# Kernel tuning notes

Measured on AMD Instinct MI355X. Metric: run time of the kernel, lower is better.

## Reference

```python
import jax, jax.numpy as jnp
import numpy as np

B, N, D, HID, S, NH = 2, 384, 768, 256, 64, 8


def layernorm(x, g, b, eps=1e-5):
    m = x.mean(-1, keepdims=True)
    v = ((x - m) ** 2).mean(-1, keepdims=True)
    return (x - m) * jax.lax.rsqrt(v + eps) * g + b


def setup_inputs() -> dict:
    key = jax.random.key(0)
    ks = jax.random.split(key, 32)
    r = lambda i, shp: jax.random.normal(ks[i], shp, dtype=jnp.float32) * 0.02
    inp = {
        'coordinates': jax.random.normal(ks[0], (B, N, 3), dtype=jnp.float32),
        'features': jax.random.normal(ks[1], (B, N, D), dtype=jnp.float32),
        'superpoint_labels': jax.random.randint(ks[2], (B, N), 0, S),
        # geometric_encoder: Linear(9,HID)-LN-ReLU-Linear(HID,D)-LN
        'ge_w1': r(3, (9, HID)), 'ge_b1': jnp.zeros((HID,)),
        'ge_g1': jnp.ones((HID,)), 'ge_be1': jnp.zeros((HID,)),
        'ge_w2': r(4, (HID, D)), 'ge_b2': jnp.zeros((D,)),
        'ge_g2': jnp.ones((D,)), 'ge_be2': jnp.zeros((D,)),
        # superpoint_aggregator: Linear(D,HID)-LN-ReLU-Linear(HID,D)-LN
        'ag_w1': r(5, (D, HID)), 'ag_b1': jnp.zeros((HID,)),
        'ag_g1': jnp.ones((HID,)), 'ag_be1': jnp.zeros((HID,)),
        'ag_w2': r(6, (HID, D)), 'ag_b2': jnp.zeros((D,)),
        'ag_g2': jnp.ones((D,)), 'ag_be2': jnp.zeros((D,)),
        # spatial_attention (MultiheadAttention, 8 heads)
        'wq': r(7, (D, D)), 'bq': jnp.zeros((D,)),
        'wk': r(8, (D, D)), 'bk': jnp.zeros((D,)),
        'wv': r(9, (D, D)), 'bv': jnp.zeros((D,)),
        'wo': r(10, (D, D)), 'bo': jnp.zeros((D,)),
    }
    return inp


def _forward(coordinates, features, superpoint_labels,
             ge_w1, ge_b1, ge_g1, ge_be1, ge_w2, ge_b2, ge_g2, ge_be2,
             ag_w1, ag_b1, ag_g1, ag_be1, ag_w2, ag_b2, ag_g2, ag_be2,
             wq, bq, wk, bk, wv, bv, wo, bo):
    # pairwise geometric relations: [B,N,N,9]
    rp = coordinates[:, :, None, :] - coordinates[:, None, :, :]
    dist = jnp.linalg.norm(rp, axis=-1, keepdims=True)
    rn = rp / jnp.maximum(dist, 1e-12)  # F.normalize semantics
    z = jnp.zeros_like(rn[..., 0])
    # torch loop writes channels (i*3+j-3): (0,1)->-2==3, (0,2)->-1==4, (1,2)->2; ch 0,1 stay zero
    ang = jnp.stack([z, z, rn[..., 1] * rn[..., 2],
                     rn[..., 0] * rn[..., 1], rn[..., 0] * rn[..., 2]], axis=-1)
    rel = jnp.concatenate([dist, rn, ang], axis=-1)
    h = jax.nn.relu(layernorm(rel @ ge_w1 + ge_b1, ge_g1, ge_be1))
    enc = layernorm(h @ ge_w2 + ge_b2, ge_g2, ge_be2)  # [B,N,N,D]
    geo_ctx = enc.mean(axis=2)  # [B,N,D]
    # per-superpoint scatter-mean (vectorized over all groups)
    oh = jax.nn.one_hot(superpoint_labels, S, dtype=features.dtype)  # [B,N,S]
    cnt = oh.sum(axis=1)  # [B,S]
    denom = jnp.maximum(cnt, 1.0)[..., None]
    mean_f = jnp.einsum('bns,bnd->bsd', oh, features) / denom
    mean_g = jnp.einsum('bns,bnd->bsd', oh, geo_ctx) / denom
    ah = jax.nn.relu(layernorm(mean_f @ ag_w1 + ag_b1, ag_g1, ag_be1))
    agg = layernorm(ah @ ag_w2 + ag_b2, ag_g2, ag_be2)
    combined = agg + mean_g  # [B,S,D]
    bidx = jnp.arange(B)[:, None]
    comb_g = combined[bidx, superpoint_labels]  # gather back [B,N,D]
    valid = (cnt[bidx, superpoint_labels] >= 2.0)[..., None]
    cw = 0.3  # consistency_weight
    enhanced = jnp.where(valid, (1.0 - cw) * features + cw * comb_g, features)
    # cross-attention: q=enhanced, k=v=geo_ctx
    dh = D // NH
    q = (enhanced @ wq + bq).reshape(B, N, NH, dh).transpose(0, 2, 1, 3)
    k = (geo_ctx @ wk + bk).reshape(B, N, NH, dh).transpose(0, 2, 1, 3)
    v = (geo_ctx @ wv + bv).reshape(B, N, NH, dh).transpose(0, 2, 1, 3)
    attn = jax.nn.softmax(jnp.einsum('bhqd,bhkd->bhqk', q, k) * (dh ** -0.5), axis=-1)
    o = jnp.einsum('bhqk,bhkd->bhqd', attn, v).transpose(0, 2, 1, 3).reshape(B, N, D)
    spatial = o @ wo + bo
    return enhanced + 0.5 * spatial


def reference(coordinates, features, superpoint_labels,
              ge_w1, ge_b1, ge_g1, ge_be1, ge_w2, ge_b2, ge_g2, ge_be2,
              ag_w1, ag_b1, ag_g1, ag_be1, ag_w2, ag_b2, ag_g2, ag_be2,
              wq, bq, wk, bk, wv, bv, wo, bo):
    return _forward(coordinates, features, superpoint_labels,
                    ge_w1, ge_b1, ge_g1, ge_be1, ge_w2, ge_b2, ge_g2, ge_be2,
                    ag_w1, ag_b1, ag_g1, ag_be1, ag_w2, ag_b2, ag_g2, ag_be2,
                    wq, bq, wk, bk, wv, bv, wo, bo)
```

## Files before the change

### kernel.cpp

```cpp
#include <hip/hip_runtime.h>
#include <hip/hip_bf16.h>
#include <stdint.h>
#include <stddef.h>

#define BB 2
#define NN 384
#define DD 768
#define HH 256
#define SS 64
#define NHH 8
#define DHH 96

typedef __attribute__((ext_vector_type(8))) short bf16x8;
typedef __attribute__((ext_vector_type(4))) float f32x4;

__device__ __forceinline__ float bits_f(unsigned short u){
  unsigned x = ((unsigned)u) << 16; float f; __builtin_memcpy(&f, &x, 4); return f;
}
__device__ __forceinline__ unsigned short f_bits(float a){
  unsigned x; __builtin_memcpy(&x, &a, 4);
  unsigned r = x + 0x7fffu + ((x >> 16) & 1u);
  return (unsigned short)(r >> 16);
}
__device__ __forceinline__ float lo_f(unsigned u){ unsigned x = u << 16; float f; __builtin_memcpy(&f,&x,4); return f; }
__device__ __forceinline__ float hi_f(unsigned u){ unsigned x = u & 0xffff0000u; float f; __builtin_memcpy(&f,&x,4); return f; }

__global__ __launch_bounds__(256) void k_prep(
    const float* __restrict__ w2, const float* __restrict__ w1g,
    const float* __restrict__ wq, const float* __restrict__ wk,
    const float* __restrict__ wv, const float* __restrict__ wo,
    const float* __restrict__ aw1, const float* __restrict__ aw2,
    float* __restrict__ zf, short* __restrict__ w2T, short* __restrict__ w2r,
    short* __restrict__ wqT, short* __restrict__ wkT, short* __restrict__ wvT,
    short* __restrict__ woT, short* __restrict__ w1t,
    short* __restrict__ agw1T, short* __restrict__ agw2T)
{
  __shared__ short tile[64*66];
  const int tid = threadIdx.x, blk = blockIdx.x;
  if (blk < 1549){
    int idx = blk*256 + tid;
    if (idx < 396416) zf[idx] = 0.f;
    return;
  }
  if (blk < 1597){
    int t = blk - 1549;
    int r0 = (t/12)*64, c0 = (t%12)*64;
    int g = tid >> 6, c = tid & 63;
    #pragma unroll
    for (int i=0;i<16;++i){
      int r = i*4 + g;
      tile[r*66 + c] = (short)f_bits(w2[(size_t)(r0+r)*768 + c0 + c]);
    }
    __syncthreads();
    #pragma unroll
    for (int i=0;i<16;++i){
      int cc = i*4 + g, rr = c;
      w2T[(size_t)(c0+cc)*256 + r0 + rr] = tile[rr*66 + cc];
    }
    return;
  }
  if (blk < 2365){
    int idx = (blk-1597)*256 + tid;
    w2r[idx] = (short)f_bits(w2[idx]);
    return;
  }
  if (blk < 2941){
    int t = blk - 2365;
    int mat = t / 144, tt = t % 144;
    const float* W = (mat==0)?wq:(mat==1)?wk:(mat==2)?wv:wo;
    short* T = (mat==0)?wqT:(mat==1)?wkT:(mat==2)?wvT:woT;
    int r0 = (tt/12)*64, c0 = (tt%12)*64;
    int g = tid >> 6, c = tid & 63;
    #pragma unroll
    for (int i=0;i<16;++i){
      int r = i*4 + g;
      tile[r*66 + c] = (short)f_bits(W[(size_t)(r0+r)*768 + c0 + c]);
    }
    __syncthreads();
    #pragma unroll
    for (int i=0;i<16;++i){
      int cc = i*4 + g, rr = c;
      T[(size_t)(c0+cc)*768 + r0 + rr] = tile[rr*66 + cc];
    }
    return;
  }
  if (blk < 2973){
    int idx = (blk-2941)*256 + tid;
    int c = idx >> 5, kk = idx & 31;
    w1t[idx] = (kk < 9) ? (short)f_bits(w1g[kk*256 + c]) : (short)0;
    return;
  }
  if (blk < 3021){
    int t = blk - 2973;
    int r0 = (t/4)*64, c0 = (t%4)*64;
    int g = tid >> 6, c = tid & 63;
    #pragma unroll
    for (int i=0;i<16;++i){
      int r = i*4 + g;
      tile[r*66 + c] = (short)f_bits(aw1[(size_t)(r0+r)*256 + c0 + c]);
    }
    __syncthreads();
    #pragma unroll
    for (int i=0;i<16;++i){
      int cc = i*4 + g, rr = c;
      agw1T[(size_t)(c0+cc)*768 + r0 + rr] = tile[rr*66 + cc];
    }
    return;
  }
  {
    int t = blk - 3021;
    int r0 = (t/12)*64, c0 = (t%12)*64;
    int g = tid >> 6, c = tid & 63;
    #pragma unroll
    for (int i=0;i<16;++i){
      int r = i*4 + g;
      tile[r*66 + c] = (short)f_bits(aw2[(size_t)(r0+r)*768 + c0 + c]);
    }
    __syncthreads();
    #pragma unroll
    for (int i=0;i<16;++i){
      int cc = i*4 + g, rr = c;
      agw2T[(size_t)(c0+cc)*256 + r0 + rr] = tile[rr*66 + cc];
    }
  }
}

__global__ __launch_bounds__(256) void k_gprep(const short* __restrict__ w2r,
                                               const float* __restrict__ b2,
                                               const short* __restrict__ w1t,
                                               const float* __restrict__ b1,
                                               short* __restrict__ Gm, float* __restrict__ gscal,
                                               float* __restrict__ g1s){
  __shared__ float b2s[768];
  __shared__ float red[8];
  const int tid = threadIdx.x, blk = blockIdx.x;
  if (blk < 64){
    const int wave = tid >> 6, lane = tid & 63, quad = lane >> 4, l16 = lane & 15;
    const int id = blk*4 + wave, ti = id >> 4, tj = id & 15;
    f32x4 acc = (f32x4){0.f,0.f,0.f,0.f};
    for (int ks = 0; ks < 24; ++ks){
      bf16x8 af = *(const bf16x8*)&w2r[(size_t)(ti*16 + l16)*768 + ks*32 + quad*8];
      bf16x8 bf = *(const bf16x8*)&w2r[(size_t)(tj*16 + l16)*768 + ks*32 + quad*8];
      acc = __builtin_amdgcn_mfma_f32_16x16x32_bf16(af, bf, acc, 0,0,0);
    }
    #pragma unroll
    for (int r = 0; r < 4; ++r)
      Gm[(ti*16 + quad*4 + r)*256 + tj*16 + l16] = (short)f_bits(acc[r]);
  } else if (blk == 64){
    for (int c = tid; c < 768; c += 256) b2s[c] = b2[c];
    __syncthreads();
    float sa = 0.f, wa = 0.f;
    const uint4* wr = (const uint4*)(w2r + (size_t)tid*768);
    #pragma unroll 4
    for (int kk = 0; kk < 96; ++kk){
      uint4 ww = wr[kk];
      const float* bp = &b2s[kk*8];
      float x0=lo_f(ww.x), x1=hi_f(ww.x), x2=lo_f(ww.y), x3=hi_f(ww.y);
      float x4=lo_f(ww.z), x5=hi_f(ww.z), x6=lo_f(ww.w), x7=hi_f(ww.w);
      sa += (x0+x1)+(x2+x3)+(x4+x5)+(x6+x7);
      wa += bp[0]*x0 + bp[1]*x1 + bp[2]*x2 + bp[3]*x3
          + bp[4]*x4 + bp[5]*x5 + bp[6]*x6 + bp[7]*x7;
    }
    Gm[256*256 + tid] = (short)f_bits(sa);
    Gm[257*256 + tid] = (short)f_bits(wa);
    #pragma unroll
    for (int rr = 258; rr < 288; ++rr) Gm[rr*256 + tid] = 0;
    float pb = 0.f, pbb = 0.f;
    for (int c = tid; c < 768; c += 256){ float bb = b2s[c]; pb += bb; pbb += bb*bb; }
    for (int m = 32; m >= 1; m >>= 1){ pb += __shfl_xor(pb,m); pbb += __shfl_xor(pbb,m); }
    if ((tid & 63) == 0){ red[tid>>6] = pb; red[4+(tid>>6)] = pbb; }
    __syncthreads();
    if (tid == 0){ gscal[0] = red[0]+red[1]+red[2]+red[3]; gscal[1] = red[4]+red[5]+red[6]+red[7]; }
  } else {
    const unsigned short* w1u = (const unsigned short*)w1t;
    if (tid < 81){
      int i = tid / 9, j = tid % 9;
      float acc = 0.f;
      for (int c = 0; c < 256; ++c)
        acc += bits_f(w1u[c*32 + i]) * bits_f(w1u[c*32 + j]);
      g1s[18 + tid] = acc;
    } else if (tid < 90){
      int i = tid - 81;
      float sa = 0.f, sb = 0.f;
      for (int c = 0; c < 256; ++c){
        float x = bits_f(w1u[c*32 + i]);
        sa += x; sb += x * b1[c];
      }
      g1s[i] = sa; g1s[9 + i] = sb;
    } else if (tid == 90){
      float pb = 0.f, pbb = 0.f;
      for (int c = 0; c < 256; ++c){ float bb = b1[c]; pb += bb; pbb += bb*bb; }
      g1s[99] = pb; g1s[100] = pbb;
    }
  }
}

__global__ __launch_bounds__(256, 3) void k_geo(
    const float* __restrict__ coord, const short* __restrict__ w1t,
    const float* __restrict__ b1g, const float* __restrict__ g1g, const float* __restrict__ be1g,
    const short* __restrict__ Gm, const float* __restrict__ gscal,
    const float* __restrict__ g1s, float* __restrict__ gv)
{
  __shared__ short relbf[64*36];
  __shared__ short h_bf[64*256];
  __shared__ float rmean[64], rrstd[64];
  __shared__ float msum[64], wbsum[64], qsum[64];

  const int tid = threadIdx.x;
  const int pair = blockIdx.x % 768;
  const int jt   = blockIdx.x / 768;
  const int j0 = jt * 64;
  const int b = pair / NN;

  if (tid < 64){
    int j = j0 + tid;
    float cix = coord[pair*3+0], ciy = coord[pair*3+1], ciz = coord[pair*3+2];
    float dx = cix - coord[(b*NN+j)*3+0];
    float dy = ciy - coord[(b*NN+j)*3+1];
    float dz = ciz - coord[(b*NN+j)*3+2];
    float dist = sqrtf(dx*dx + dy*dy + dz*dz);
    float inv = 1.f / fmaxf(dist, 1e-12f);
    float x = dx*inv, y = dy*inv, z = dz*inv;
    float rv[9];
    rv[0]=dist; rv[1]=x; rv[2]=y; rv[3]=z; rv[4]=0.f; rv[5]=0.f;
    rv[6]=y*z; rv[7]=x*y; rv[8]=x*z;
    short* rr = &relbf[tid*36];
    float rbf[9];
    #pragma unroll
    for (int k=0;k<9;++k){
      unsigned short hb = f_bits(rv[k]);
      rr[k] = (short)hb; rbf[k] = bits_f(hb);
    }
    #pragma unroll
    for (int k=9;k<32;++k) rr[k]=0;
    float s = g1s[99], ssq = g1s[100];
    #pragma unroll
    for (int i=0;i<9;++i){
      s += rbf[i]*g1s[i];
      ssq += 2.f*rbf[i]*g1s[9+i];
      #pragma unroll
      for (int jj=0;jj<9;++jj) ssq += rbf[i]*rbf[jj]*g1s[18+i*9+jj];
    }
    float mean = s*(1.f/256.f);
    float var  = ssq*(1.f/256.f) - mean*mean;
    rmean[tid] = mean; rrstd[tid] = rsqrtf(var + 1e-5f);
  } else if (tid < 128){
    qsum[tid-64] = 0.f;
  }
  __syncthreads();

  const int wave = tid >> 6, lane = tid & 63, quad = lane >> 4, l16 = lane & 15;

  {
    bf16x8 af[4];
    #pragma unroll
    for (int rb=0;rb<4;++rb)
      af[rb] = *(const bf16x8*)&relbf[(rb*16 + l16)*36 + quad*8];
    f32x4 hacc[4][4];
    #pragma unroll
    for (int ci=0;ci<4;++ci){
      int cb = wave*4 + ci;
      bf16x8 bfw = *(const bf16x8*)&w1t[(cb*16 + l16)*32 + quad*8];
      #pragma unroll
      for (int rb=0;rb<4;++rb)
        hacc[ci][rb] = __builtin_amdgcn_mfma_f32_16x16x32_bf16(af[rb], bfw, (f32x4){0.f,0.f,0.f,0.f}, 0,0,0);
    }
    f32x4 rmv[4], rsv[4];
    #pragma unroll
    for (int rb=0;rb<4;++rb){
      rmv[rb] = *(const f32x4*)&rmean[rb*16 + quad*4];
      rsv[rb] = *(const f32x4*)&rrstd[rb*16 + quad*4];
    }
    #pragma unroll
    for (int ci=0;ci<4;++ci){
      int col = (wave*4+ci)*16 + l16;
      float b1c = b1g[col], g1c = g1g[col], be1c = be1g[col];
      int chb = col >> 3, lo = col & 7;
      #pragma unroll
      for (int rb=0;rb<4;++rb){
        #pragma unroll
        for (int r=0;r<4;++r){
          int row = rb*16 + quad*4 + r;
          float hn = (hacc[ci][rb][r] + b1c - rmv[rb][r]) * rsv[rb][r] * g1c + be1c;
          h_bf[row*256 + ((chb + row)&31)*8 + lo] = (short)f_bits(fmaxf(hn, 0.f));
        }
      }
    }
  }
  __syncthreads();

  {
    f32x4 acc[4][4];
    #pragma unroll
    for (int ci=0;ci<4;++ci)
      #pragma unroll
      for (int rb=0;rb<4;++rb) acc[ci][rb] = (f32x4){0.f,0.f,0.f,0.f};
    f32x4 eacc[4];
    #pragma unroll
    for (int rb=0;rb<4;++rb) eacc[rb] = (f32x4){0.f,0.f,0.f,0.f};
    for (int ks=0;ks<8;++ks){
      bf16x8 a4[4];
      #pragma unroll
      for (int rb=0;rb<4;++rb){
        int row = rb*16 + l16;
        a4[rb] = *(const bf16x8*)&h_bf[row*256 + (((ks*4 + quad) + row)&31)*8];
      }
      #pragma unroll
      for (int ci=0;ci<4;++ci){
        int n = (wave*4+ci)*16 + l16;
        bf16x8 bg = *(const bf16x8*)&Gm[n*256 + ks*32 + quad*8];
        #pragma unroll
        for (int rb=0;rb<4;++rb)
          acc[ci][rb] = __builtin_amdgcn_mfma_f32_16x16x32_bf16(a4[rb], bg, acc[ci][rb], 0,0,0);
      }
      if (wave == 0){
        bf16x8 bge = *(const bf16x8*)&Gm[(256 + l16)*256 + ks*32 + quad*8];
        #pragma unroll
        for (int rb=0;rb<4;++rb)
          eacc[rb] = __builtin_amdgcn_mfma_f32_16x16x32_bf16(a4[rb], bge, eacc[rb], 0,0,0);
      }
    }
    if (wave == 0 && l16 < 2){
      float* dst = (l16 == 0) ? msum : wbsum;
      #pragma unroll
      for (int rb=0;rb<4;++rb)
        #pragma unroll
        for (int r=0;r<4;++r) dst[rb*16 + quad*4 + r] = eacc[rb][r];
    }
    #pragma unroll
    for (int rb=0;rb<4;++rb){
      #pragma unroll
      for (int r=0;r<4;++r){
        int row = rb*16 + quad*4 + r;
        float qp = 0.f;
        #pragma unroll
        for (int ci=0;ci<4;++ci){
          int col = (wave*4+ci)*16 + l16;
          float hv = bits_f((unsigned short)h_bf[row*256 + (((col>>3)+row)&31)*8 + (col&7)]);
          qp += acc[ci][rb][r] * hv;
        }
        qp += __shfl_xor(qp,1);
        qp += __shfl_xor(qp,2);
        qp += __shfl_xor(qp,4);
        qp += __shfl_xor(qp,8);
        if (l16 == 0) atomicAdd(&qsum[row], qp);
      }
    }
  }
  __syncthreads();
  if (tid < 64){
    float Sb = gscal[0], Sbb = gscal[1];
    float m2 = (msum[tid] + Sb)*(1.f/768.f);
    float ssq = qsum[tid] + 2.f*wbsum[tid] + Sbb;
    float var = ssq*(1.f/768.f) - m2*m2;
    rmean[tid] = m2; rrstd[tid] = rsqrtf(var + 1e-5f);
  }
  __syncthreads();
  if (tid < 64){
    float rr = rrstd[tid], tt = rmean[tid]*rrstd[tid];
    for (int m = 32; m >= 1; m >>= 1){ rr += __shfl_xor(rr,m); tt += __shfl_xor(tt,m); }
    if (tid == 0){
      atomicAdd(&gv[pair*260 + 256], rr);
      atomicAdd(&gv[pair*260 + 257], tt);
    }
  }
  {
    const int cg = tid >> 3, jg = tid & 7;
    float vacc[8];
    #pragma unroll
    for (int e=0;e<8;++e) vacc[e] = 0.f;
    #pragma unroll
    for (int jj = 0; jj < 8; ++jj){
      int j = jg*8 + jj;
      bf16x8 hv8 = *(const bf16x8*)&h_bf[j*256 + ((cg + j)&31)*8];
      float r = rrstd[j];
      #pragma unroll
      for (int e=0;e<8;++e) vacc[e] += r * bits_f((unsigned short)hv8[e]);
    }
    #pragma unroll
    for (int e=0;e<8;++e){
      vacc[e] += __shfl_xor(vacc[e],1);
      vacc[e] += __shfl_xor(vacc[e],2);
      vacc[e] += __shfl_xor(vacc[e],4);
    }
    if (jg == 0){
      #pragma unroll
      for (int e=0;e<8;++e) atomicAdd(&gv[pair*260 + cg*8 + e], vacc[e]);
    }
  }
}

__global__ __launch_bounds__(256) void k_geoscat(
    const float* __restrict__ gv, const short* __restrict__ w2r,
    const float* __restrict__ b2g, const float* __restrict__ g2g,
    const float* __restrict__ be2g, unsigned short* __restrict__ geo,
    const int* __restrict__ lab, const float* __restrict__ feat,
    float* __restrict__ mf, float* __restrict__ mg, float* __restrict__ cntw){
  __shared__ float V[256];
  __shared__ float RT[2];
  const int tid = threadIdx.x, pair = blockIdx.x;
  V[tid] = gv[pair*260 + tid];
  if (tid < 2) RT[tid] = gv[pair*260 + 256 + tid];
  __syncthreads();
  float R = RT[0], T = RT[1];
  const unsigned short* wr = (const unsigned short*)w2r;
  float a0 = 0.f, a1 = 0.f, a2 = 0.f;
  #pragma unroll 4
  for (int k = 0; k < 256; ++k){
    float vk = V[k];
    const unsigned short* row = wr + (size_t)k*768;
    a0 += vk * bits_f(row[tid]);
    a1 += vk * bits_f(row[tid+256]);
    a2 += vk * bits_f(row[tid+512]);
  }
  size_t base = (size_t)pair*DD;
  unsigned short r0 = f_bits(g2g[tid]    *(a0 + b2g[tid]    *R - T)*(1.f/384.f) + be2g[tid]);
  unsigned short r1 = f_bits(g2g[tid+256]*(a1 + b2g[tid+256]*R - T)*(1.f/384.f) + be2g[tid+256]);
  unsigned short r2 = f_bits(g2g[tid+512]*(a2 + b2g[tid+512]*R - T)*(1.f/384.f) + be2g[tid+512]);
  geo[base + tid]       = r0;
  geo[base + tid + 256] = r1;
  geo[base + tid + 512] = r2;
  const int b = pair / NN;
  const int s = lab[pair];
  const size_t sb = (size_t)(b*SS + s)*DD;
  if (tid == 0) atomicAdd(&cntw[b*SS + s], 1.0f);
  atomicAdd(&mf[sb + tid],       feat[base + tid]);
  atomicAdd(&mf[sb + tid + 256], feat[base + tid + 256]);
  atomicAdd(&mf[sb + tid + 512], feat[base + tid + 512]);
  atomicAdd(&mg[sb + tid],       bits_f(r0));
  atomicAdd(&mg[sb + tid + 256], bits_f(r1));
  atomicAdd(&mg[sb + tid + 512], bits_f(r2));
}

__global__ __launch_bounds__(256) void k_agg(
    const float* __restrict__ mf, const float* __restrict__ mg,
    const float* __restrict__ cntw,
    const short* __restrict__ w1T, const float* __restrict__ b1g,
    const float* __restrict__ g1g, const float* __restrict__ be1g,
    const short* __restrict__ w2T, const float* __restrict__ b2g,
    const float* __restrict__ g2g, const float* __restrict__ be2g,
    float* __restrict__ comb)
{
  __shared__ float xr[DD];
  __shared__ float hr[HH];
  __shared__ float red[8];
  const int tid = threadIdx.x;
  const size_t base = (size_t)blockIdx.x * DD;
  const float inv = 1.f / fmaxf(cntw[blockIdx.x], 1.f);
  for (int c = tid; c < DD; c += 256) xr[c] = mf[base + c]*inv;
  __syncthreads();
  float a = b1g[tid];
  {
    const uint4* wr = (const uint4*)(w1T + (size_t)tid*768);
    #pragma unroll 4
    for (int kk = 0; kk < 96; ++kk){
      uint4 ww = wr[kk];
      const float* xp = &xr[kk*8];
      a += xp[0]*lo_f(ww.x) + xp[1]*hi_f(ww.x)
         + xp[2]*lo_f(ww.y) + xp[3]*hi_f(ww.y)
         + xp[4]*lo_f(ww.z) + xp[5]*hi_f(ww.z)
         + xp[6]*lo_f(ww.w) + xp[7]*hi_f(ww.w);
    }
  }
  float s = a, q = a*a;
  for (int m = 32; m >= 1; m >>= 1){ s += __shfl_xor(s,m); q += __shfl_xor(q,m); }
  if ((tid & 63) == 0){ red[tid>>6] = s; red[4+(tid>>6)] = q; }
  __syncthreads();
  s = red[0]+red[1]+red[2]+red[3]; q = red[4]+red[5]+red[6]+red[7];
  float mean = s*(1.f/HH), var = q*(1.f/HH) - mean*mean, rstd = rsqrtf(var + 1e-5f);
  float h = fmaxf((a-mean)*rstd*g1g[tid] + be1g[tid], 0.f);
  hr[tid] = h;
  __syncthreads();
  float a2[3];
  #pragma unroll
  for (int u = 0; u < 3; ++u){
    int c = tid + 256*u;
    float t = b2g[c];
    const uint4* wr = (const uint4*)(w2T + (size_t)c*256);
    #pragma unroll 4
    for (int kk = 0; kk < 32; ++kk){
      uint4 ww = wr[kk];
      const float* hp = &hr[kk*8];
      t += hp[0]*lo_f(ww.x) + hp[1]*hi_f(ww.x)
         + hp[2]*lo_f(ww.y) + hp[3]*hi_f(ww.y)
         + hp[4]*lo_f(ww.z) + hp[5]*hi_f(ww.z)
         + hp[6]*lo_f(ww.w) + hp[7]*hi_f(ww.w);
    }
    a2[u] = t;
  }
  float s2 = a2[0]+a2[1]+a2[2], q2 = a2[0]*a2[0]+a2[1]*a2[1]+a2[2]*a2[2];
  for (int m = 32; m >= 1; m >>= 1){ s2 += __shfl_xor(s2,m); q2 += __shfl_xor(q2,m); }
  __syncthreads();
  if ((tid & 63) == 0){ red[tid>>6] = s2; red[4+(tid>>6)] = q2; }
  __syncthreads();
  s2 = red[0]+red[1]+red[2]+red[3]; q2 = red[4]+red[5]+red[6]+red[7];
  float mean2 = s2*(1.f/DD), rstd2 = rsqrtf(q2*(1.f/DD) - mean2*mean2 + 1e-5f);
  #pragma unroll
  for (int u = 0; u < 3; ++u){
    int c = tid + 256*u;
    comb[base + c] = (a2[u]-mean2)*rstd2*g2g[c] + be2g[c] + mg[base + c]*inv;
  }
}

__global__ void k_enhance(const float* __restrict__ feat, const int* __restrict__ lab,
                          const float* __restrict__ cntw, const float* __restrict__ comb,
                          float* __restrict__ enh, unsigned short* __restrict__ enhb)
{
  int idx = blockIdx.x * 256 + threadIdx.x;
  int c = idx % DD; int bn = idx / DD; int b = bn / NN;
  int l = lab[bn];
  float f = feat[idx];
  float cg = comb[(size_t)(b*SS + l)*DD + c];
  float cnt = cntw[b*SS + l];
  float e = (cnt >= 2.0f) ? (0.7f*f + 0.3f*cg) : f;
  enh[idx] = e;
  enhb[idx] = f_bits(e);
}

__global__ __launch_bounds__(256, 4) void k_qkv(
    const unsigned short* __restrict__ enhb, const unsigned short* __restrict__ geo,
    const short* __restrict__ wqT, const short* __restrict__ wkT, const short* __restrict__ wvT,
    const float* __restrict__ bq, const float* __restrict__ bk, const float* __restrict__ bv,
    unsigned short* __restrict__ qo, unsigned short* __restrict__ ko, unsigned short* __restrict__ vo)
{
  const int tid = threadIdx.x, blk = blockIdx.x;
  const int m = blk / 144, rem = blk % 144;
  const int rt = rem / 3, ct = rem % 3;
  const int wave = tid >> 6, lane = tid & 63, quad = lane >> 4, l16 = lane & 15;
  const short* WT = (m==0)?wqT:(m==1)?wkT:wvT;
  const float* Bv = (m==0)?bq:(m==1)?bk:bv;
  unsigned short* Y = (m==0)?qo:(m==1)?ko:vo;
  const short* X = (const short*)((m==0)? enhb : geo);
  const float oscale = (m==0)? 0.10206207261596577f : 1.0f;
  const int row0 = rt*16;
  const int col0 = ct*256 + wave*64;

  f32x4 acc[4];
  #pragma unroll
  for (int cb=0;cb<4;++cb) acc[cb] = (f32x4){0.f,0.f,0.f,0.f};
  for (int ks = 0; ks < 24; ++ks){
    bf16x8 af = *(const bf16x8*)&X[(size_t)(row0 + l16)*DD + ks*32 + quad*8];
    #pragma unroll
    for (int cb=0;cb<4;++cb){
      bf16x8 bw = *(const bf16x8*)&WT[(size_t)(col0 + cb*16 + l16)*DD + ks*32 + quad*8];
      acc[cb] = __builtin_amdgcn_mfma_f32_16x16x32_bf16(af, bw, acc[cb], 0,0,0);
    }
  }
  #pragma unroll
  for (int cb=0;cb<4;++cb){
    int col = col0 + cb*16 + l16;
    float bb = Bv[col];
    #pragma unroll
    for (int r=0;r<4;++r){
      int row = row0 + quad*4 + r;
      Y[(size_t)row*DD + col] = f_bits((acc[cb][r] + bb)*oscale);
    }
  }
}

__global__ __launch_bounds__(256) void k_attn_split(
    const unsigned short* __restrict__ qws, const unsigned short* __restrict__ kws,
    const unsigned short* __restrict__ vws, float* __restrict__ pws)
{
  __shared__ short kt[64*104];
  __shared__ short vt[64*104];
  __shared__ float st[32*66];
  __shared__ float lsum[32];
  const int tid = threadIdx.x;
  const int half = blockIdx.x / 192;
  const int inner = blockIdx.x % 192;
  const int b = inner / (NHH*12); int rem = inner % (NHH*12);
  const int h = rem / 12; const int qt = rem % 12; const int q0 = qt*32;
  const int sq = tid >> 3, jp = tid & 7;
  const int qp = tid >> 4, dp = tid & 15;
  unsigned qreg[48];
  {
    const unsigned* qr = (const unsigned*)(qws + (size_t)(b*NN + q0 + sq)*DD + h*DHH);
    #pragma unroll
    for (int d2 = 0; d2 < 48; ++d2) qreg[d2] = qr[d2];
  }
  if (tid < 32) lsum[tid] = 0.f;
  float Oacc[2][6];
  #pragma unroll
// ... 153 lines not shown
      }
    }
  }
  __syncthreads();
  float l0 = 1.f / lsum[2*qp], l1 = 1.f / lsum[2*qp+1];
  size_t ob = (size_t)(b*NN + q0)*DD + h*DHH + dp*6;
  #pragma unroll
  for (int m = 0; m < 6; ++m){
    ows[ob + (size_t)(2*qp)*DD + m]   = f_bits(Oacc[0][m]*l0);
    ows[ob + (size_t)(2*qp+1)*DD + m] = f_bits(Oacc[1][m]*l1);
  }
}

__global__ __launch_bounds__(256, 4) void k_out(
    const unsigned short* __restrict__ ows, const float* __restrict__ enh,
    const short* __restrict__ woT, const float* __restrict__ bo, float* __restrict__ out)
{
  const int tid = threadIdx.x, blk = blockIdx.x;
  const int rt = blk / 3, ct = blk % 3;
  const int wave = tid >> 6, lane = tid & 63, quad = lane >> 4, l16 = lane & 15;
  const int row0 = rt*16;
  const int col0 = ct*256 + wave*64;
  f32x4 acc[4];
  #pragma unroll
  for (int cb=0;cb<4;++cb) acc[cb] = (f32x4){0.f,0.f,0.f,0.f};
  for (int ks = 0; ks < 24; ++ks){
    bf16x8 af = *(const bf16x8*)&((const short*)ows)[(size_t)(row0 + l16)*DD + ks*32 + quad*8];
    #pragma unroll
    for (int cb=0;cb<4;++cb){
      bf16x8 bw = *(const bf16x8*)&woT[(size_t)(col0 + cb*16 + l16)*DD + ks*32 + quad*8];
      acc[cb] = __builtin_amdgcn_mfma_f32_16x16x32_bf16(af, bw, acc[cb], 0,0,0);
    }
  }
  #pragma unroll
  for (int cb=0;cb<4;++cb){
    int col = col0 + cb*16 + l16;
    float bb = bo[col];
    #pragma unroll
    for (int r=0;r<4;++r){
      size_t idx = (size_t)(row0 + quad*4 + r)*DD + col;
      out[idx] = enh[idx] + 0.5f*(acc[cb][r] + bb);
    }
  }
}

extern "C" void kernel_launch(void* const* d_in, const int* in_sizes, int n_in,
                              void* d_out, int out_size, void* d_ws, size_t ws_size,
                              hipStream_t stream) {
  const float* coord = (const float*)d_in[0];
  const float* feat  = (const float*)d_in[1];
  const int*   lab   = (const int*)d_in[2];
  const float* ge_w1 = (const float*)d_in[3];
  const float* ge_b1 = (const float*)d_in[4];
  const float* ge_g1 = (const float*)d_in[5];
  const float* ge_be1= (const float*)d_in[6];
  const float* ge_w2 = (const float*)d_in[7];
  const float* ge_b2 = (const float*)d_in[8];
  const float* ge_g2 = (const float*)d_in[9];
  const float* ge_be2= (const float*)d_in[10];
  const float* ag_w1 = (const float*)d_in[11];
  const float* ag_b1 = (const float*)d_in[12];
  const float* ag_g1 = (const float*)d_in[13];
  const float* ag_be1= (const float*)d_in[14];
  const float* ag_w2 = (const float*)d_in[15];
  const float* ag_b2 = (const float*)d_in[16];
  const float* ag_g2 = (const float*)d_in[17];
  const float* ag_be2= (const float*)d_in[18];
  const float* wq = (const float*)d_in[19];
  const float* bq = (const float*)d_in[20];
  const float* wk = (const float*)d_in[21];
  const float* bk = (const float*)d_in[22];
  const float* wv = (const float*)d_in[23];
  const float* bv = (const float*)d_in[24];
  const float* wo = (const float*)d_in[25];
  const float* bo = (const float*)d_in[26];

  char* w = (char*)d_ws;
  unsigned short* geo_bf = (unsigned short*)(w);
  float*          enh_f  = (float*)(w + 1179648);
  unsigned short* enh_bf = (unsigned short*)(w + 3538944);
  unsigned short* qw_bf  = (unsigned short*)(w + 4718592);
  unsigned short* kw_bf  = (unsigned short*)(w + 5898240);
  unsigned short* vw_bf  = (unsigned short*)(w + 7077888);
  float*          gv     = (float*)(w + 8257536);
  float*          mf     = (float*)(w + 9056256);
  float*          mg     = (float*)(w + 9449472);
  float*          cntw   = (float*)(w + 9842688);
  float*          comb   = (float*)(w + 9843200);
  short*          w2T    = (short*)(w + 10236416);
  short*          w2r    = (short*)(w + 10629632);
  short*          w1t    = (short*)(w + 11022848);
  short*          Gm     = (short*)(w + 11039232);
  float*          g1s    = (float*)(w + 11186688);
  float*          gscal  = (float*)(w + 11187200);
  short*          wqT    = (short*)(w + 11187456);
  short*          wkT    = (short*)(w + 12367104);
  short*          wvT    = (short*)(w + 13546752);
  short*          woT    = (short*)(w + 14726400);
  short*          agw1T  = (short*)(w + 15906048);
  short*          agw2T  = (short*)(w + 16299264);
  float*          pws    = (float*)(w + 16692480);
  unsigned short* ow_bf  = geo_bf;
  const bool split_attn = (ws_size >= 21460224);

  hipLaunchKernelGGL(k_prep,    dim3(3069),  dim3(256), 0, stream,
                     ge_w2, ge_w1, wq, wk, wv, wo, ag_w1, ag_w2,
                     gv, w2T, w2r, wqT, wkT, wvT, woT, w1t, agw1T, agw2T);
  hipLaunchKernelGGL(k_gprep,   dim3(66),    dim3(256), 0, stream,
                     w2r, ge_b2, w1t, ge_b1, Gm, gscal, g1s);
  hipLaunchKernelGGL(k_geo,     dim3(4608),  dim3(256), 0, stream,
                     coord, w1t, ge_b1, ge_g1, ge_be1, Gm, gscal, g1s, gv);
  hipLaunchKernelGGL(k_geoscat, dim3(768),   dim3(256), 0, stream,
                     gv, w2r, ge_b2, ge_g2, ge_be2, geo_bf, lab, feat, mf, mg, cntw);
  hipLaunchKernelGGL(k_agg,     dim3(128),   dim3(256), 0, stream,
                     mf, mg, cntw, agw1T, ag_b1, ag_g1, ag_be1, agw2T, ag_b2, ag_g2, ag_be2, comb);
  hipLaunchKernelGGL(k_enhance, dim3(2304),  dim3(256), 0, stream,
                     feat, lab, cntw, comb, enh_f, enh_bf);
  hipLaunchKernelGGL(k_qkv,     dim3(432),   dim3(256), 0, stream,
                     enh_bf, geo_bf, wqT, wkT, wvT, bq, bk, bv, qw_bf, kw_bf, vw_bf);
  if (split_attn){
    hipLaunchKernelGGL(k_attn_split, dim3(384), dim3(256), 0, stream,
                       qw_bf, kw_bf, vw_bf, pws);
    hipLaunchKernelGGL(k_attnfin,    dim3(192), dim3(256), 0, stream,
                       pws, ow_bf);
  } else {
    hipLaunchKernelGGL(k_attn_full,  dim3(192), dim3(256), 0, stream,
                       qw_bf, kw_bf, vw_bf, ow_bf);
  }
  hipLaunchKernelGGL(k_out,     dim3(144),   dim3(256), 0, stream,
                     ow_bf, enh_f, woT, bo, (float*)d_out);
}
```

Baseline: 426.9 us.

## Fuse geo scatter into k_geo, replace atomic superpoint sums with gather in k_agg

k_geo now runs one block per point pair-row and loops over all six j-tiles inside the block, keeping the reductions in registers and shared memory. It then applies the w2 projection and LayerNorm directly, which removes the gv zero-fill, the global atomics and the separate k_geoscat launch. k_agg now builds the per-superpoint feature and geo means itself by scanning the labels, replacing the atomic scatter into mf/mg/cntw. The cost is fewer blocks for k_geo (768 instead of 4608), which lowers parallelism, and a serial scan over 384 points in each k_agg block.

Result: slower. 922.7 us (+116.2%).

```diff
diff --git a/kernel.cpp b/kernel.cpp
--- a/kernel.cpp
+++ b/kernel.cpp
@@ -30,20 +30,15 @@
     const float* __restrict__ wq, const float* __restrict__ wk,
     const float* __restrict__ wv, const float* __restrict__ wo,
     const float* __restrict__ aw1, const float* __restrict__ aw2,
-    float* __restrict__ zf, short* __restrict__ w2T, short* __restrict__ w2r,
+    short* __restrict__ w2T, short* __restrict__ w2r,
     short* __restrict__ wqT, short* __restrict__ wkT, short* __restrict__ wvT,
     short* __restrict__ woT, short* __restrict__ w1t,
     short* __restrict__ agw1T, short* __restrict__ agw2T)
 {
   __shared__ short tile[64*66];
   const int tid = threadIdx.x, blk = blockIdx.x;
-  if (blk < 1549){
-    int idx = blk*256 + tid;
-    if (idx < 396416) zf[idx] = 0.f;
-    return;
-  }
-  if (blk < 1597){
-    int t = blk - 1549;
+  if (blk < 48){
+    int t = blk;
     int r0 = (t/12)*64, c0 = (t%12)*64;
     int g = tid >> 6, c = tid & 63;
     #pragma unroll
@@ -59,13 +54,13 @@
     }
     return;
   }
-  if (blk < 2365){
-    int idx = (blk-1597)*256 + tid;
+  if (blk < 816){
+    int idx = (blk-48)*256 + tid;
     w2r[idx] = (short)f_bits(w2[idx]);
     return;
   }
-  if (blk < 2941){
-    int t = blk - 2365;
+  if (blk < 1392){
+    int t = blk - 816;
     int mat = t / 144, tt = t % 144;
     const float* W = (mat==0)?wq:(mat==1)?wk:(mat==2)?wv:wo;
     short* T = (mat==0)?wqT:(mat==1)?wkT:(mat==2)?wvT:woT;
@@ -84,14 +79,14 @@
     }
     return;
   }
-  if (blk < 2973){
-    int idx = (blk-2941)*256 + tid;
+  if (blk < 1424){
+    int idx = (blk-1392)*256 + tid;
     int c = idx >> 5, kk = idx & 31;
     w1t[idx] = (kk < 9) ? (short)f_bits(w1g[kk*256 + c]) : (short)0;
     return;
   }
-  if (blk < 3021){
-    int t = blk - 2973;
+  if (blk < 1472){
+    int t = blk - 1424;
     int r0 = (t/4)*64, c0 = (t%4)*64;
     int g = tid >> 6, c = tid & 63;
     #pragma unroll
@@ -108,7 +103,7 @@
     return;
   }
   {
-    int t = blk - 3021;
+    int t = blk - 1472;
     int r0 = (t/12)*64, c0 = (t%12)*64;
     int g = tid >> 6, c = tid & 63;
     #pragma unroll
@@ -199,176 +194,179 @@
     const float* __restrict__ coord, const short* __restrict__ w1t,
     const float* __restrict__ b1g, const float* __restrict__ g1g, const float* __restrict__ be1g,
     const short* __restrict__ Gm, const float* __restrict__ gscal,
-    const float* __restrict__ g1s, float* __restrict__ gv)
+    const float* __restrict__ g1s, const short* __restrict__ w2r,
+    const float* __restrict__ b2g, const float* __restrict__ g2g,
+    const float* __restrict__ be2g, unsigned short* __restrict__ geo)
 {
   __shared__ short relbf[64*36];
   __shared__ short h_bf[64*256];
   __shared__ float rmean[64], rrstd[64];
   __shared__ float msum[64], wbsum[64], qsum[64];
+  __shared__ float Vsh[256];
+  __shared__ float RT[2];
 
   const int tid = threadIdx.x;
-  const int pair = blockIdx.x % 768;
-  const int jt   = blockIdx.x / 768;
-  const int j0 = jt * 64;
+  const int pair = blockIdx.x;
   const int b = pair / NN;
-
+  const int wave = tid >> 6, lane = tid & 63, quad = lane >> 4, l16 = lane & 15;
+  const int cg = tid >> 3, jg = tid & 7;
+
+  float cix = 0.f, ciy = 0.f, ciz = 0.f;
   if (tid < 64){
-    int j = j0 + tid;
-    float cix = coord[pair*3+0], ciy = coord[pair*3+1], ciz = coord[pair*3+2];
-    float dx = cix - coord[(b*NN+j)*3+0];
-    float dy = ciy - coord[(b*NN+j)*3+1];
-    float dz = ciz - coord[(b*NN+j)*3+2];
-    float dist = sqrtf(dx*dx + dy*dy + dz*dz);
-    float inv = 1.f / fmaxf(dist, 1e-12f);
-    float x = dx*inv, y = dy*inv, z = dz*inv;
-    float rv[9];
-    rv[0]=dist; rv[1]=x; rv[2]=y; rv[3]=z; rv[4]=0.f; rv[5]=0.f;
-    rv[6]=y*z; rv[7]=x*y; rv[8]=x*z;
-    short* rr = &relbf[tid*36];
-    float rbf[9];
-    #pragma unroll
-    for (int k=0;k<9;++k){
-      unsigned short hb = f_bits(rv[k]);
-      rr[k] = (short)hb; rbf[k] = bits_f(hb);
-    }
-    #pragma unroll
-    for (int k=9;k<32;++k) rr[k]=0;
-    float s = g1s[99], ssq = g1s[100];
-    #pragma unroll
-    for (int i=0;i<9;++i){
-      s += rbf[i]*g1s[i];
-      ssq += 2.f*rbf[i]*g1s[9+i];
-      #pragma unroll
-      for (int jj=0;jj<9;++jj) ssq += rbf[i]*rbf[jj]*g1s[18+i*9+jj];
-    }
-    float mean = s*(1.f/256.f);
-    float var  = ssq*(1.f/256.f) - mean*mean;
-    rmean[tid] = mean; rrstd[tid] = rsqrtf(var + 1e-5f);
-  } else if (tid < 128){
-    qsum[tid-64] = 0.f;
-  }
-  __syncthreads();
-
-  const int wave = tid >> 6, lane = tid & 63, quad = lane >> 4, l16 = lane & 15;
-
-  {
-    bf16x8 af[4];
-    #pragma unroll
-    for (int rb=0;rb<4;++rb)
-      af[rb] = *(const bf16x8*)&relbf[(rb*16 + l16)*36 + quad*8];
-    f32x4 hacc[4][4];
-    #pragma unroll
-    for (int ci=0;ci<4;++ci){
-      int cb = wave*4 + ci;
-      bf16x8 bfw = *(const bf16x8*)&w1t[(cb*16 + l16)*32 + quad*8];
+    cix = coord[pair*3+0]; ciy = coord[pair*3+1]; ciz = coord[pair*3+2];
+  }
+  const float Sb = gscal[0], Sbb = gscal[1];
+  float vacc[8];
+  #pragma unroll
+  for (int e=0;e<8;++e) vacc[e] = 0.f;
+  float Racc = 0.f, Tacc = 0.f;
+
+  for (int jt = 0; jt < 6; ++jt){
+    const int j0 = jt * 64;
+    if (tid < 64){
+      int j = j0 + tid;
+      float dx = cix - coord[(b*NN+j)*3+0];
+      float dy = ciy - coord[(b*NN+j)*3+1];
+      float dz = ciz - coord[(b*NN+j)*3+2];
+      float dist = sqrtf(dx*dx + dy*dy + dz*dz);
+      float inv = 1.f / fmaxf(dist, 1e-12f);
+      float x = dx*inv, y = dy*inv, z = dz*inv;
+      float rv[9];
+      rv[0]=dist; rv[1]=x; rv[2]=y; rv[3]=z; rv[4]=0.f; rv[5]=0.f;
+      rv[6]=y*z; rv[7]=x*y; rv[8]=x*z;
+      short* rr = &relbf[tid*36];
+      float rbf[9];
+      #pragma unroll
+      for (int k=0;k<9;++k){
+        unsigned short hb = f_bits(rv[k]);
+        rr[k] = (short)hb; rbf[k] = bits_f(hb);
+      }
+      #pragma unroll
+      for (int k=9;k<32;++k) rr[k]=0;
+      float s = g1s[99], ssq = g1s[100];
+      #pragma unroll
+      for (int i=0;i<9;++i){
+        s += rbf[i]*g1s[i];
+        ssq += 2.f*rbf[i]*g1s[9+i];
+        #pragma unroll
+        for (int jj=0;jj<9;++jj) ssq += rbf[i]*rbf[jj]*g1s[18+i*9+jj];
+      }
+      float mean = s*(1.f/256.f);
+      float var  = ssq*(1.f/256.f) - mean*mean;
+      rmean[tid] = mean; rrstd[tid] = rsqrtf(var + 1e-5f);
+    } else if (tid < 128){
+      qsum[tid-64] = 0.f;
+    }
+    __syncthreads();
+
+    {
+      bf16x8 af[4];
       #pragma unroll
       for (int rb=0;rb<4;++rb)
-        hacc[ci][rb] = __builtin_amdgcn_mfma_f32_16x16x32_bf16(af[rb], bfw, (f32x4){0.f,0.f,0.f,0.f}, 0,0,0);
-    }
-    f32x4 rmv[4], rsv[4];
-    #pragma unroll
-    for (int rb=0;rb<4;++rb){
-      rmv[rb] = *(const f32x4*)&rmean[rb*16 + quad*4];
-      rsv[rb] = *(const f32x4*)&rrstd[rb*16 + quad*4];
-    }
-    #pragma unroll
-    for (int ci=0;ci<4;++ci){
-      int col = (wave*4+ci)*16 + l16;
-      float b1c = b1g[col], g1c = g1g[col], be1c = be1g[col];
-      int chb = col >> 3, lo = col & 7;
+        af[rb] = *(const bf16x8*)&relbf[(rb*16 + l16)*36 + quad*8];
+      f32x4 hacc[4][4];
+      #pragma unroll
+      for (int ci=0;ci<4;++ci){
+        int cb = wave*4 + ci;
+        bf16x8 bfw = *(const bf16x8*)&w1t[(cb*16 + l16)*32 + quad*8];
+        #pragma unroll
+        for (int rb=0;rb<4;++rb)
+          hacc[ci][rb] = __builtin_amdgcn_mfma_f32_16x16x32_bf16(af[rb], bfw, (f32x4){0.f,0.f,0.f,0.f}, 0,0,0);
+      }
+      f32x4 rmv[4], rsv[4];
+      #pragma unroll
+      for (int rb=0;rb<4;++rb){
+        rmv[rb] = *(const f32x4*)&rmean[rb*16 + quad*4];
+        rsv[rb] = *(const f32x4*)&rrstd[rb*16 + quad*4];
+      }
+      #pragma unroll
+      for (int ci=0;ci<4;++ci){
+        int col = (wave*4+ci)*16 + l16;
+        float b1c = b1g[col], g1c = g1g[col], be1c = be1g[col];
+        int chb = col >> 3, lo = col & 7;
+        #pragma unroll
+        for (int rb=0;rb<4;++rb){
+          #pragma unroll
+          for (int r=0;r<4;++r){
+            int row = rb*16 + quad*4 + r;
+            float hn = (hacc[ci][rb][r] + b1c - rmv[rb][r]) * rsv[rb][r] * g1c + be1c;
+            h_bf[row*256 + ((chb + row)&31)*8 + lo] = (short)f_bits(fmaxf(hn, 0.f));
+          }
+        }
+      }
+    }
+    __syncthreads();
+
+    {
+      f32x4 acc[4][4];
+      #pragma unroll
+      for (int ci=0;ci<4;++ci)
+        #pragma unroll
+        for (int rb=0;rb<4;++rb) acc[ci][rb] = (f32x4){0.f,0.f,0.f,0.f};
+      f32x4 eacc[4];
+      #pragma unroll
+      for (int rb=0;rb<4;++rb) eacc[rb] = (f32x4){0.f,0.f,0.f,0.f};
+      for (int ks=0;ks<8;++ks){
+        bf16x8 a4[4];
+        #pragma unroll
+        for (int rb=0;rb<4;++rb){
+          int row = rb*16 + l16;
+          a4[rb] = *(const bf16x8*)&h_bf[row*256 + (((ks*4 + quad) + row)&31)*8];
+        }
+        #pragma unroll
+        for (int ci=0;ci<4;++ci){
+          int n = (wave*4+ci)*16 + l16;
+          bf16x8 bg = *(const bf16x8*)&Gm[n*256 + ks*32 + quad*8];
+          #pragma unroll
+          for (int rb=0;rb<4;++rb)
+            acc[ci][rb] = __builtin_amdgcn_mfma_f32_16x16x32_bf16(a4[rb], bg, acc[ci][rb], 0,0,0);
+        }
+        if (wave == 0){
+          bf16x8 bge = *(const bf16x8*)&Gm[(256 + l16)*256 + ks*32 + quad*8];
+          #pragma unroll
+          for (int rb=0;rb<4;++rb)
+            eacc[rb] = __builtin_amdgcn_mfma_f32_16x16x32_bf16(a4[rb], bge, eacc[rb], 0,0,0);
+        }
+      }
+      if (wave == 0 && l16 < 2){
+        float* dst = (l16 == 0) ? msum : wbsum;
+        #pragma unroll
+        for (int rb=0;rb<4;++rb)
+          #pragma unroll
+          for (int r=0;r<4;++r) dst[rb*16 + quad*4 + r] = eacc[rb][r];
+      }
       #pragma unroll
       for (int rb=0;rb<4;++rb){
         #pragma unroll
         for (int r=0;r<4;++r){
           int row = rb*16 + quad*4 + r;
-          float hn = (hacc[ci][rb][r] + b1c - rmv[rb][r]) * rsv[rb][r] * g1c + be1c;
-          h_bf[row*256 + ((chb + row)&31)*8 + lo] = (short)f_bits(fmaxf(hn, 0.f));
+          float qp = 0.f;
+          #pragma unroll
+          for (int ci=0;ci<4;++ci){
+            int col = (wave*4+ci)*16 + l16;
+            float hv = bits_f((unsigned short)h_bf[row*256 + (((col>>3)+row)&31)*8 + (col&7)]);
+            qp += acc[ci][rb][r] * hv;
+          }
+          qp += __shfl_xor(qp,1);
+          qp += __shfl_xor(qp,2);
+          qp += __shfl_xor(qp,4);
+          qp += __shfl_xor(qp,8);
+          if (l16 == 0) atomicAdd(&qsum[row], qp);
         }
       }
     }
-  }
-  __syncthreads();
-
-  {
-    f32x4 acc[4][4];
-    #pragma unroll
-    for (int ci=0;ci<4;++ci)
-      #pragma unroll
-      for (int rb=0;rb<4;++rb) acc[ci][rb] = (f32x4){0.f,0.f,0.f,0.f};
-    f32x4 eacc[4];
-    #pragma unroll
-    for (int rb=0;rb<4;++rb) eacc[rb] = (f32x4){0.f,0.f,0.f,0.f};
-    for (int ks=0;ks<8;++ks){
-      bf16x8 a4[4];
-      #pragma unroll
-      for (int rb=0;rb<4;++rb){
-        int row = rb*16 + l16;
-        a4[rb] = *(const bf16x8*)&h_bf[row*256 + (((ks*4 + quad) + row)&31)*8];
-      }
-      #pragma unroll
-      for (int ci=0;ci<4;++ci){
-        int n = (wave*4+ci)*16 + l16;
-        bf16x8 bg = *(const bf16x8*)&Gm[n*256 + ks*32 + quad*8];
-        #pragma unroll
-        for (int rb=0;rb<4;++rb)
-          acc[ci][rb] = __builtin_amdgcn_mfma_f32_16x16x32_bf16(a4[rb], bg, acc[ci][rb], 0,0,0);
-      }
-      if (wave == 0){
-        bf16x8 bge = *(const bf16x8*)&Gm[(256 + l16)*256 + ks*32 + quad*8];
-        #pragma unroll
-        for (int rb=0;rb<4;++rb)
-          eacc[rb] = __builtin_amdgcn_mfma_f32_16x16x32_bf16(a4[rb], bge, eacc[rb], 0,0,0);
-      }
-    }
-    if (wave == 0 && l16 < 2){
-      float* dst = (l16 == 0) ? msum : wbsum;
-      #pragma unroll
-      for (int rb=0;rb<4;++rb)
-        #pragma unroll
-        for (int r=0;r<4;++r) dst[rb*16 + quad*4 + r] = eacc[rb][r];
-    }
-    #pragma unroll
-    for (int rb=0;rb<4;++rb){
-      #pragma unroll
-      for (int r=0;r<4;++r){
-        int row = rb*16 + quad*4 + r;
-        float qp = 0.f;
-        #pragma unroll
-        for (int ci=0;ci<4;++ci){
-          int col = (wave*4+ci)*16 + l16;
-          float hv = bits_f((unsigned short)h_bf[row*256 + (((col>>3)+row)&31)*8 + (col&7)]);
-          qp += acc[ci][rb][r] * hv;
-        }
-        qp += __shfl_xor(qp,1);
-        qp += __shfl_xor(qp,2);
-        qp += __shfl_xor(qp,4);
-        qp += __shfl_xor(qp,8);
-        if (l16 == 0) atomicAdd(&qsum[row], qp);
-      }
-    }
-  }
-  __syncthreads();
-  if (tid < 64){
-    float Sb = gscal[0], Sbb = gscal[1];
-    float m2 = (msum[tid] + Sb)*(1.f/768.f);
-    float ssq = qsum[tid] + 2.f*wbsum[tid] + Sbb;
-    float var = ssq*(1.f/768.f) - m2*m2;
-    rmean[tid] = m2; rrstd[tid] = rsqrtf(var + 1e-5f);
-  }
-  __syncthreads();
-  if (tid < 64){
-    float rr = rrstd[tid], tt = rmean[tid]*rrstd[tid];
-    for (int m = 32; m >= 1; m >>= 1){ rr += __shfl_xor(rr,m); tt += __shfl_xor(tt,m); }
-    if (tid == 0){
-      atomicAdd(&gv[pair*260 + 256], rr);
-      atomicAdd(&gv[pair*260 + 257], tt);
-    }
-  }
-  {
-    const int cg = tid >> 3, jg = tid & 7;
-    float vacc[8];
-    #pragma unroll
-    for (int e=0;e<8;++e) vacc[e] = 0.f;
+    __syncthreads();
+
+    if (tid < 64){
+      float m2 = (msum[tid] + Sb)*(1.f/768.f);
+      float ssq = qsum[tid] + 2.f*wbsum[tid] + Sbb;
+      float var = ssq*(1.f/768.f) - m2*m2;
+      float rs = rsqrtf(var + 1e-5f);
+      rrstd[tid] = rs;
+      Racc += rs; Tacc += m2*rs;
+    }
+    __syncthreads();
+
     #pragma unroll
     for (int jj = 0; jj < 8; ++jj){
       int j = jg*8 + jj;
@@ -377,77 +375,79 @@
       #pragma unroll
       for (int e=0;e<8;++e) vacc[e] += r * bits_f((unsigned short)hv8[e]);
     }
-    #pragma unroll
-    for (int e=0;e<8;++e){
-      vacc[e] += __shfl_xor(vacc[e],1);
-      vacc[e] += __shfl_xor(vacc[e],2);
-      vacc[e] += __shfl_xor(vacc[e],4);
-    }
-    if (jg == 0){
-      #pragma unroll
-      for (int e=0;e<8;++e) atomicAdd(&gv[pair*260 + cg*8 + e], vacc[e]);
-    }
-  }
-}
-
-__global__ __launch_bounds__(256) void k_geoscat(
-    const float* __restrict__ gv, const short* __restrict__ w2r,
-    const float* __restrict__ b2g, const float* __restrict__ g2g,
-    const float* __restrict__ be2g, unsigned short* __restrict__ geo,
-    const int* __restrict__ lab, const float* __restrict__ feat,
-    float* __restrict__ mf, float* __restrict__ mg, float* __restrict__ cntw){
-  __shared__ float V[256];
-  __shared__ float RT[2];
-  const int tid = threadIdx.x, pair = blockIdx.x;
-  V[tid] = gv[pair*260 + tid];
-  if (tid < 2) RT[tid] = gv[pair*260 + 256 + tid];
-  __syncthreads();
-  float R = RT[0], T = RT[1];
+    __syncthreads();
+  }
+
+  #pragma unroll
+  for (int e=0;e<8;++e){
+    vacc[e] += __shfl_xor(vacc[e],1);
+    vacc[e] += __shfl_xor(vacc[e],2);
+    vacc[e] += __shfl_xor(vacc[e],4);
+  }
+  if (jg == 0){
+    #pragma unroll
+    for (int e=0;e<8;++e) Vsh[cg*8 + e] = vacc[e];
+  }
+  if (tid < 64){
+    for (int m = 32; m >= 1; m >>= 1){ Racc += __shfl_xor(Racc,m); Tacc += __shfl_xor(Tacc,m); }
+    if (tid == 0){ RT[0] = Racc; RT[1] = Tacc; }
+  }
+  __syncthreads();
+
+  const float R = RT[0], T = RT[1];
   const unsigned short* wr = (const unsigned short*)w2r;
   float a0 = 0.f, a1 = 0.f, a2 = 0.f;
   #pragma unroll 4
   for (int k = 0; k < 256; ++k){
-    float vk = V[k];
+    float vk = Vsh[k];
     const unsigned short* row = wr + (size_t)k*768;
     a0 += vk * bits_f(row[tid]);
     a1 += vk * bits_f(row[tid+256]);
     a2 += vk * bits_f(row[tid+512]);
   }
   size_t base = (size_t)pair*DD;
-  unsigned short r0 = f_bits(g2g[tid]    *(a0 + b2g[tid]    *R - T)*(1.f/384.f) + be2g[tid]);
-  unsigned short r1 = f_bits(g2g[tid+256]*(a1 + b2g[tid+256]*R - T)*(1.f/384.f) + be2g[tid+256]);
-  unsigned short r2 = f_bits(g2g[tid+512]*(a2 + b2g[tid+512]*R - T)*(1.f/384.f) + be2g[tid+512]);
-  geo[base + tid]       = r0;
-  geo[base + tid + 256] = r1;
-  geo[base + tid + 512] = r2;
-  const int b = pair / NN;
-  const int s = lab[pair];
-  const size_t sb = (size_t)(b*SS + s)*DD;
-  if (tid == 0) atomicAdd(&cntw[b*SS + s], 1.0f);
-  atomicAdd(&mf[sb + tid],       feat[base + tid]);
-  atomicAdd(&mf[sb + tid + 256], feat[base + tid + 256]);
-  atomicAdd(&mf[sb + tid + 512], feat[base + tid + 512]);
-  atomicAdd(&mg[sb + tid],       bits_f(r0));
-  atomicAdd(&mg[sb + tid + 256], bits_f(r1));
-  atomicAdd(&mg[sb + tid + 512], bits_f(r2));
+  geo[base + tid]       = f_bits(g2g[tid]    *(a0 + b2g[tid]    *R - T)*(1.f/384.f) + be2g[tid]);
+  geo[base + tid + 256] = f_bits(g2g[tid+256]*(a1 + b2g[tid+256]*R - T)*(1.f/384.f) + be2g[tid+256]);
+  geo[base + tid + 512] = f_bits(g2g[tid+512]*(a2 + b2g[tid+512]*R - T)*(1.f/384.f) + be2g[tid+512]);
 }
 
 __global__ __launch_bounds__(256) void k_agg(
-    const float* __restrict__ mf, const float* __restrict__ mg,
-    const float* __restrict__ cntw,
+    const int* __restrict__ lab, const float* __restrict__ feat,
+    const unsigned short* __restrict__ geo, float* __restrict__ cntw,
     const short* __restrict__ w1T, const float* __restrict__ b1g,
     const float* __restrict__ g1g, const float* __restrict__ be1g,
     const short* __restrict__ w2T, const float* __restrict__ b2g,
     const float* __restrict__ g2g, const float* __restrict__ be2g,
     float* __restrict__ comb)
 {
+  __shared__ int ls[NN];
   __shared__ float xr[DD];
   __shared__ float hr[HH];
   __shared__ float red[8];
   const int tid = threadIdx.x;
-  const size_t base = (size_t)blockIdx.x * DD;
-  const float inv = 1.f / fmaxf(cntw[blockIdx.x], 1.f);
-  for (int c = tid; c < DD; c += 256) xr[c] = mf[base + c]*inv;
+  const int bs = blockIdx.x, b = bs >> 6, s = bs & 63;
+  for (int j = tid; j < NN; j += 256) ls[j] = lab[b*NN + j];
+  __syncthreads();
+  float f0 = 0.f, f1 = 0.f, f2 = 0.f, gg0 = 0.f, gg1 = 0.f, gg2 = 0.f;
+  int cnt = 0;
+  for (int j = 0; j < NN; ++j){
+    if (ls[j] == s){
+      ++cnt;
+      size_t rb = (size_t)(b*NN + j)*DD;
+      f0  += feat[rb + tid];
+      f1  += feat[rb + tid + 256];
+      f2  += feat[rb + tid + 512];
+      gg0 += bits_f(geo[rb + tid]);
+      gg1 += bits_f(geo[rb + tid + 256]);
+      gg2 += bits_f(geo[rb + tid + 512]);
+    }
+  }
+  const float inv = 1.f / fmaxf((float)cnt, 1.f);
+  if (tid == 0) cntw[bs] = (float)cnt;
+  xr[tid]       = f0*inv;
+  xr[tid + 256] = f1*inv;
+  xr[tid + 512] = f2*inv;
+  float gmean[3] = { gg0*inv, gg1*inv, gg2*inv };
   __syncthreads();
   float a = b1g[tid];
   {
@@ -462,16 +462,16 @@
          + xp[6]*lo_f(ww.w) + xp[7]*hi_f(ww.w);
     }
   }
-  float s = a, q = a*a;
-  for (int m = 32; m >= 1; m >>= 1){ s += __shfl_xor(s,m); q += __shfl_xor(q,m); }
-  if ((tid & 63) == 0){ red[tid>>6] = s; red[4+(tid>>6)] = q; }
-  __syncthreads();
-  s = red[0]+red[1]+red[2]+red[3]; q = red[4]+red[5]+red[6]+red[7];
-  float mean = s*(1.f/HH), var = q*(1.f/HH) - mean*mean, rstd = rsqrtf(var + 1e-5f);
+  float sum1 = a, q1 = a*a;
+  for (int m = 32; m >= 1; m >>= 1){ sum1 += __shfl_xor(sum1,m); q1 += __shfl_xor(q1,m); }
+  if ((tid & 63) == 0){ red[tid>>6] = sum1; red[4+(tid>>6)] = q1; }
+  __syncthreads();
+  sum1 = red[0]+red[1]+red[2]+red[3]; q1 = red[4]+red[5]+red[6]+red[7];
+  float mean = sum1*(1.f/HH), var = q1*(1.f/HH) - mean*mean, rstd = rsqrtf(var + 1e-5f);
   float h = fmaxf((a-mean)*rstd*g1g[tid] + be1g[tid], 0.f);
   hr[tid] = h;
   __syncthreads();
-  float a2[3];
+  float y[3];
   #pragma unroll
   for (int u = 0; u < 3; ++u){
     int c = tid + 256*u;
@@ -486,19 +486,20 @@
          + hp[4]*lo_f(ww.z) + hp[5]*hi_f(ww.z)
          + hp[6]*lo_f(ww.w) + hp[7]*hi_f(ww.w);
     }
-    a2[u] = t;
-  }
-  float s2 = a2[0]+a2[1]+a2[2], q2 = a2[0]*a2[0]+a2[1]*a2[1]+a2[2]*a2[2];
+    y[u] = t;
+  }
+  float s2 = y[0]+y[1]+y[2], q2 = y[0]*y[0]+y[1]*y[1]+y[2]*y[2];
   for (int m = 32; m >= 1; m >>= 1){ s2 += __shfl_xor(s2,m); q2 += __shfl_xor(q2,m); }
   __syncthreads();
   if ((tid & 63) == 0){ red[tid>>6] = s2; red[4+(tid>>6)] = q2; }
   __syncthreads();
   s2 = red[0]+red[1]+red[2]+red[3]; q2 = red[4]+red[5]+red[6]+red[7];
   float mean2 = s2*(1.f/DD), rstd2 = rsqrtf(q2*(1.f/DD) - mean2*mean2 + 1e-5f);
+  size_t base = (size_t)bs * DD;
   #pragma unroll
   for (int u = 0; u < 3; ++u){
     int c = tid + 256*u;
-    comb[base + c] = (a2[u]-mean2)*rstd2*g2g[c] + be2g[c] + mg[base + c]*inv;
+    comb[base + c] = (y[u]-mean2)*rstd2*g2g[c] + be2g[c] + gmean[u];
   }
 }
 
@@ -818,9 +819,6 @@
   unsigned short* qw_bf  = (unsigned short*)(w + 4718592);
   unsigned short* kw_bf  = (unsigned short*)(w + 5898240);
   unsigned short* vw_bf  = (unsigned short*)(w + 7077888);
-  float*          gv     = (float*)(w + 8257536);
-  float*          mf     = (float*)(w + 9056256);
-  float*          mg     = (float*)(w + 9449472);
   float*          cntw   = (float*)(w + 9842688);
   float*          comb   = (float*)(w + 9843200);
   short*          w2T    = (short*)(w + 10236416);
@@ -839,17 +837,17 @@
   unsigned short* ow_bf  = geo_bf;
   const bool split_attn = (ws_size >= 21460224);
 
-  hipLaunchKernelGGL(k_prep,    dim3(3069),  dim3(256), 0, stream,
+  hipLaunchKernelGGL(k_prep,    dim3(1520),  dim3(256), 0, stream,
                      ge_w2, ge_w1, wq, wk, wv, wo, ag_w1, ag_w2,
-                     gv, w2T, w2r, wqT, wkT, wvT, woT, w1t, agw1T, agw2T);
+                     w2T, w2r, wqT, wkT, wvT, woT, w1t, agw1T, agw2T);
   hipLaunchKernelGGL(k_gprep,   dim3(66),    dim3(256), 0, stream,
                      w2r, ge_b2, w1t, ge_b1, Gm, gscal, g1s);
-  hipLaunchKernelGGL(k_geo,     dim3(4608),  dim3(256), 0, stream,
-                     coord, w1t, ge_b1, ge_g1, ge_be1, Gm, gscal, g1s, gv);
-  hipLaunchKernelGGL(k_geoscat, dim3(768),   dim3(256), 0, stream,
-                     gv, w2r, ge_b2, ge_g2, ge_be2, geo_bf, lab, feat, mf, mg, cntw);
+  hipLaunchKernelGGL(k_geo,     dim3(768),   dim3(256), 0, stream,
+                     coord, w1t, ge_b1, ge_g1, ge_be1, Gm, gscal, g1s,
+                     w2r, ge_b2, ge_g2, ge_be2, geo_bf);
   hipLaunchKernelGGL(k_agg,     dim3(128),   dim3(256), 0, stream,
-                     mf, mg, cntw, agw1T, ag_b1, ag_g1, ag_be1, agw2T, ag_b2, ag_g2, ag_be2, comb);
+                     lab, feat, geo_bf, cntw, agw1T, ag_b1, ag_g1, ag_be1,
+                     agw2T, ag_b2, ag_g2, ag_be2, comb);
   hipLaunchKernelGGL(k_enhance, dim3(2304),  dim3(256), 0, stream,
                      feat, lab, cntw, comb, enh_f, enh_bf);
   hipLaunchKernelGGL(k_qkv,     dim3(432),   dim3(256), 0, stream,
```
